# Optimization experiments

Hardware: AMD Instinct MI355X
Metric: run time of the kernel (lower is better)

The kernel has to match this reference:

```python
import jax, jax.numpy as jnp
import numpy as np

N_NODES = 50000
N_EDGES = 800000
D = 64
VOCAB = 1000
NUM_ITERS = 2
BN_EPS = 1e-5


def _bn(h, g, b):
    # BatchNorm1d in training mode: batch statistics over the edge dim, biased var
    mu = h.mean(axis=0)
    var = h.var(axis=0)
    return g * (h - mu) * jax.lax.rsqrt(var + BN_EPS) + b


def _edge_agg(x, idx_i, idx_j, W1, b1, g1, be1, W2, b2, g2, be2):
    # gather -> concat -> Linear+BN+ReLU x2 -> scatter-sum to idx_i -> degree norm
    m = jnp.concatenate([x[idx_i], x[idx_j]], axis=1)          # [E, 2D]
    h = jax.nn.relu(_bn(m @ W1 + b1, g1, be1))                  # [E, D]
    h = jax.nn.relu(_bn(h @ W2 + b2, g2, be2))                  # [E, D]
    agg = jax.ops.segment_sum(h, idx_i, num_segments=N_NODES)   # [N, D]
    deg = jax.ops.segment_sum(jnp.ones((idx_i.shape[0],), x.dtype), idx_i,
                              num_segments=N_NODES)
    deg_inv = jnp.where(deg > 0, 1.0 / deg, 0.0)
    return deg_inv[:, None] * agg


def setup_inputs() -> dict:
    key = jax.random.key(0)
    ks = jax.random.split(key, 24)
    s = 0.05
    inp = {
        'nodes': jax.random.randint(ks[0], (N_NODES,), 0, VOCAB),
        'edges': jax.random.randint(ks[1], (2, N_EDGES), 0, N_NODES),
        'emb': jax.random.normal(ks[2], (VOCAB, D), jnp.float32) * s,
        # parent aggregation MLP
        'p_W1': jax.random.normal(ks[3], (2 * D, D), jnp.float32) * s,
        'p_b1': jnp.zeros((D,), jnp.float32),
        'p_g1': jnp.ones((D,), jnp.float32),
        'p_be1': jnp.zeros((D,), jnp.float32),
        'p_W2': jax.random.normal(ks[4], (D, D), jnp.float32) * s,
        'p_b2': jnp.zeros((D,), jnp.float32),
        'p_g2': jnp.ones((D,), jnp.float32),
        'p_be2': jnp.zeros((D,), jnp.float32),
        # child aggregation MLP
        'c_W1': jax.random.normal(ks[5], (2 * D, D), jnp.float32) * s,
        'c_b1': jnp.zeros((D,), jnp.float32),
        'c_g1': jnp.ones((D,), jnp.float32),
        'c_be1': jnp.zeros((D,), jnp.float32),
        'c_W2': jax.random.normal(ks[6], (D, D), jnp.float32) * s,
        'c_b2': jnp.zeros((D,), jnp.float32),
        'c_g2': jnp.ones((D,), jnp.float32),
        'c_be2': jnp.zeros((D,), jnp.float32),
        # final aggregation (dropout = identity, eval semantics)
        'fc_W': jax.random.normal(ks[7], (3 * D, 2 * D), jnp.float32) * s,
        'fc_b': jnp.zeros((2 * D,), jnp.float32),
        'fc2_W': jax.random.normal(ks[8], (2 * D, D), jnp.float32) * s,
        'fc2_b': jnp.zeros((D,), jnp.float32),
        # Conv1d(D, 2D, kernel=1) == Linear D -> 2D
        'conv_W': jax.random.normal(ks[9], (D, 2 * D), jnp.float32) * s,
        'conv_b': jnp.zeros((2 * D,), jnp.float32),
    }
    return inp


def reference(nodes, edges, emb, p_W1, p_b1, p_g1, p_be1, p_W2, p_b2, p_g2, p_be2,
              c_W1, c_b1, c_g1, c_be1, c_W2, c_b2, c_g2, c_be2,
              fc_W, fc_b, fc2_W, fc2_b, conv_W, conv_b):
    src, dst = edges[0], edges[1]
    x = emb[nodes]                                            # [N, D]
    for _ in range(NUM_ITERS):
        # ParentAggregation: flow source_to_target -> x_i = x[dst], x_j = x[src], scatter to dst
        fi = _edge_agg(x, dst, src, p_W1, p_b1, p_g1, p_be1, p_W2, p_b2, p_g2, p_be2)
        # ChildAggregation: flow target_to_source -> x_i = x[src], x_j = x[dst], scatter to src
        fo = _edge_agg(x, src, dst, c_W1, c_b1, c_g1, c_be1, c_W2, c_b2, c_g2, c_be2)
        cat = jnp.concatenate([x, fi, fo], axis=1)            # [N, 3D]
        upd = jax.nn.relu(cat @ fc_W + fc_b) @ fc2_W + fc2_b  # [N, D]
        x = x + upd
    return x @ conv_W + conv_b                                # [N, 2D]
```

## Files before the change

kernel.cpp:

```cpp
#include <hip/hip_runtime.h>

#define NN 50000
#define NE 800000
#define BN_EPS 1e-5f
#define SCAN_T 256
#define SCAN_NB ((NN + SCAN_T - 1) / SCAN_T)

#define BKT_SH 8
#define NBKT ((NN + 255) >> 8)
#define CAP 6144
#define PCH 4096
#define NPB ((NE + PCH - 1) / PCH)

#define ST_SUM1 0
#define ST_SQ1 64
#define ST_CROSS 128
#define ST_SUM2 192
#define ST_SSQ2 256
#define ST_AGG 320

using bf16x8 = __attribute__((ext_vector_type(8))) __bf16;
using bf16x4 = __attribute__((ext_vector_type(4))) __bf16;
using floatx4 = __attribute__((ext_vector_type(4))) float;

#define MFMA16(a, b, c) __builtin_amdgcn_mfma_f32_16x16x32_bf16(a, b, c, 0, 0, 0)

__device__ __forceinline__ bf16x8 load_wfrag(const float* W, int ncols, int kb, int ct, int lane) {
  int col = ct * 16 + (lane & 15);
  int k0 = kb * 32 + ((lane >> 4) << 3);
  bf16x8 f;
#pragma unroll
  for (int j = 0; j < 8; ++j) f[j] = (__bf16)W[(k0 + j) * ncols + col];
  return f;
}

__global__ void k_setup(const int* __restrict__ nodes, const float* __restrict__ emb,
                        float* __restrict__ x, int* __restrict__ bcur) {
  int tid = blockIdx.x * blockDim.x + threadIdx.x;
  int stride = gridDim.x * blockDim.x;
  for (int idx = tid; idx < NN * 64; idx += stride)
    x[idx] = emb[nodes[idx >> 6] * 64 + (idx & 63)];
  for (int t = tid; t < 2 * NBKT; t += stride)
    bcur[t] = (t < NBKT ? t : t - NBKT) * CAP;
}

__global__ void __launch_bounds__(256) k_part(const int* __restrict__ src,
                                              const int* __restrict__ dst,
                                              int* __restrict__ bcur,
                                              unsigned int* __restrict__ stage) {
  const int dir = blockIdx.y;
  const int* key = dir ? src : dst;
  int* bc = bcur + dir * NBKT;
  unsigned int* st = stage + (size_t)dir * NBKT * CAP;
  __shared__ int lh[256];
  __shared__ int sb[256];
  __shared__ int lbase[NBKT];
  __shared__ unsigned int pay[PCH];
  const int tid = threadIdx.x;
  lh[tid] = 0;
  __syncthreads();
  const int c0 = blockIdx.x * PCH;
  const int nv = (NE - c0 < PCH) ? (NE - c0) : PCH;
  unsigned int rk[PCH / 256];
#pragma unroll
  for (int i = 0; i < PCH / 256; ++i) {
    int l = i * 256 + tid;
    if (l < nv) {
      int b = key[c0 + l] >> BKT_SH;
      int r = atomicAdd(&lh[b], 1);
      rk[i] = ((unsigned)b << 13) | (unsigned)r;
    } else {
      rk[i] = 0xFFFFFFFFu;
    }
  }
  __syncthreads();
  int cntv = lh[tid];
  sb[tid] = cntv;
  __syncthreads();
  for (int o = 1; o < 256; o <<= 1) {
    int u = (tid >= o) ? sb[tid - o] : 0;
    __syncthreads();
    sb[tid] += u;
    __syncthreads();
  }
  int excl = sb[tid] - cntv;
  __syncthreads();
  sb[tid] = excl;
  if (tid < NBKT && cntv > 0) lbase[tid] = atomicAdd(&bc[tid], cntv);
  __syncthreads();
#pragma unroll
  for (int i = 0; i < PCH / 256; ++i) {
    if (rk[i] != 0xFFFFFFFFu) {
      int e = c0 + i * 256 + tid;
      int b = (int)(rk[i] >> 13);
      int r = (int)(rk[i] & 0x1FFFu);
      unsigned int s = (unsigned)src[e], d = (unsigned)dst[e];
      pay[sb[b] + r] = dir ? ((s << 16) | d) : ((d << 16) | s);
    }
  }
  __syncthreads();
  for (int t = tid; t < nv; t += 256) {
    int lo = 0, hi = 255;
    while (lo < hi) {
      int mid = (lo + hi + 1) >> 1;
      if (sb[mid] <= t) lo = mid; else hi = mid - 1;
    }
    st[lbase[lo] + (t - sb[lo])] = pay[t];
  }
}

__global__ void __launch_bounds__(256) k_count(const int* __restrict__ bcur,
                                               const unsigned int* __restrict__ stage,
                                               int* __restrict__ cnt_d, int* __restrict__ cnt_s) {
  const int dir = blockIdx.y;
  const int b = blockIdx.x;
  int* cnt = dir ? cnt_s : cnt_d;
  const unsigned int* st = stage + (size_t)dir * NBKT * CAP + (size_t)b * CAP;
  __shared__ int lc[256];
  lc[threadIdx.x] = 0;
  __syncthreads();
  int sz = bcur[dir * NBKT + b] - b * CAP;
  for (int t = threadIdx.x; t < sz; t += 256)
    atomicAdd(&lc[(st[t] >> 16) - (b << BKT_SH)], 1);
  __syncthreads();
  int n = (b << BKT_SH) + threadIdx.x;
  if (n < NN) cnt[n] = lc[threadIdx.x];
}

__global__ void k_scan1(const int* __restrict__ cnt_d, const int* __restrict__ cnt_s,
                        int* __restrict__ off_d, int* __restrict__ off_s, int* __restrict__ btot) {
  const int* cnt = blockIdx.y ? cnt_s : cnt_d;
  int* off = blockIdx.y ? off_s : off_d;
  __shared__ int sm[SCAN_T];
  int i = blockIdx.x * SCAN_T + threadIdx.x;
  int v = (i < NN) ? cnt[i] : 0;
  sm[threadIdx.x] = v;
  __syncthreads();
  for (int o = 1; o < SCAN_T; o <<= 1) {
    int u = (threadIdx.x >= o) ? sm[threadIdx.x - o] : 0;
    __syncthreads();
    sm[threadIdx.x] += u;
    __syncthreads();
  }
  if (i < NN) off[i] = sm[threadIdx.x];
  if (threadIdx.x == SCAN_T - 1) btot[blockIdx.y * SCAN_NB + blockIdx.x] = sm[SCAN_T - 1];
}

__global__ void k_scan2(int* __restrict__ btot) {
  __shared__ int sm[SCAN_T];
  int t = threadIdx.x;
  for (int y = 0; y < 2; ++y) {
    int v = (t < SCAN_NB) ? btot[y * SCAN_NB + t] : 0;
    sm[t] = v;
    __syncthreads();
    for (int o = 1; o < SCAN_T; o <<= 1) {
      int u = (t >= o) ? sm[t - o] : 0;
      __syncthreads();
      sm[t] += u;
      __syncthreads();
    }
    if (t < SCAN_NB) btot[y * SCAN_NB + t] = sm[t] - v;
    __syncthreads();
  }
}

__global__ void k_scan3(const int* __restrict__ cnt_d, const int* __restrict__ cnt_s,
                        int* __restrict__ off_d, int* __restrict__ off_s,
                        const int* __restrict__ btot, float* __restrict__ dinv_d,
                        float* __restrict__ dinv_s) {
  const int* cnt = blockIdx.y ? cnt_s : cnt_d;
  int* off = blockIdx.y ? off_s : off_d;
  float* dinv = blockIdx.y ? dinv_s : dinv_d;
  int i = blockIdx.x * SCAN_T + threadIdx.x;
  if (i < NN) {
    int incl = off[i];
    int c = cnt[i];
    int o = incl - c + btot[blockIdx.y * SCAN_NB + blockIdx.x];
    off[i] = o;
    dinv[i] = c > 0 ? 1.0f / (float)c : 0.f;
  }
  if (i == NN - 1) off[NN] = NE;
}

__global__ void __launch_bounds__(256) k_fill2(const int* __restrict__ bcur,
                                               const unsigned int* __restrict__ stage,
                                               const int* __restrict__ off_d,
                                               const int* __restrict__ off_s,
                                               unsigned short* __restrict__ jl_d,
                                               unsigned short* __restrict__ jl_s,
                                               unsigned short* __restrict__ il_d,
                                               unsigned short* __restrict__ il_s) {
  const int dir = blockIdx.y;
  const int b = blockIdx.x;
  const int* off = dir ? off_s : off_d;
  unsigned short* jl = dir ? jl_s : jl_d;
  unsigned short* il = dir ? il_s : il_d;
  const unsigned int* st = stage + (size_t)dir * NBKT * CAP + (size_t)b * CAP;
  __shared__ int lcur[256];
  __shared__ unsigned short ljl[CAP];
  __shared__ unsigned short lil[CAP];
  int csr0 = off[b << BKT_SH];
  int n = (b << BKT_SH) + threadIdx.x;
  lcur[threadIdx.x] = (n < NN) ? off[n] - csr0 : 0;
  __syncthreads();
  int sz = bcur[dir * NBKT + b] - b * CAP;
  for (int t = threadIdx.x; t < sz; t += 256) {
    unsigned int v = st[t];
    int p = atomicAdd(&lcur[(v >> 16) - (b << BKT_SH)], 1);
    ljl[p] = (unsigned short)(v & 0xFFFFu);
    lil[p] = (unsigned short)(v >> 16);
  }
  __syncthreads();
  for (int t = threadIdx.x; t < sz; t += 256) {
    jl[csr0 + t] = ljl[t];
    il[csr0 + t] = lil[t];
  }
}

__global__ void __launch_bounds__(256) k_node_xform(
    const float* __restrict__ x, const float* __restrict__ W1,
    __bf16* __restrict__ Ab, __bf16* __restrict__ Bb,
    float* __restrict__ stats, int do_zero) {
  const int lane = threadIdx.x & 63;
  const int wid = threadIdx.x >> 6;
  __shared__ alignas(16) __bf16 xb[4][16 * 72];
  if (do_zero && blockIdx.x == 0)
    for (int t = threadIdx.x; t < 2 * ST_AGG; t += blockDim.x) stats[t] = 0.f;
  bf16x8 wfa[4][2], wfb[4][2];
#pragma unroll
  for (int ct = 0; ct < 4; ++ct)
#pragma unroll
    for (int kb = 0; kb < 2; ++kb) {
      wfa[ct][kb] = load_wfrag(W1, 64, kb, ct, lane);
      wfb[ct][kb] = load_wfrag(W1 + 64 * 64, 64, kb, ct, lane);
    }
  __bf16* vb = xb[wid];
  int wgid = (blockIdx.x * blockDim.x + threadIdx.x) >> 6;
  int nw = (gridDim.x * blockDim.x) >> 6;
  for (int tile = wgid; tile < NN / 16; tile += nw) {
#pragma unroll
    for (int t = 0; t < 16; ++t)
      vb[t * 72 + lane] = (__bf16)x[(tile * 16 + t) * 64 + lane];
    const bf16x8 a0 = *(const bf16x8*)&vb[(lane & 15) * 72 + ((lane >> 4) << 3)];
    const bf16x8 a1 = *(const bf16x8*)&vb[(lane & 15) * 72 + 32 + ((lane >> 4) << 3)];
#pragma unroll
    for (int ct = 0; ct < 4; ++ct) {
      floatx4 aA = {0.f, 0.f, 0.f, 0.f}, aB = {0.f, 0.f, 0.f, 0.f};
      aA = MFMA16(a0, wfa[ct][0], aA);
      aA = MFMA16(a1, wfa[ct][1], aA);
      aB = MFMA16(a0, wfb[ct][0], aB);
      aB = MFMA16(a1, wfb[ct][1], aB);
#pragma unroll
      for (int r = 0; r < 4; ++r) {
        int row = ((lane >> 4) << 2) + r;
        int o = (tile * 16 + row) * 64 + ct * 16 + (lane & 15);
        Ab[o] = (__bf16)aA[r];
        Bb[o] = (__bf16)aB[r];
      }
    }
  }
}

__global__ void __launch_bounds__(256) k_node_stats(
    const __bf16* __restrict__ Ap, const __bf16* __restrict__ Bp,
    const __bf16* __restrict__ Ac, const __bf16* __restrict__ Bc,
    const int* __restrict__ cnt_d, const int* __restrict__ cnt_s,
    float* __restrict__ stats) {
  const int lane = threadIdx.x & 63;
  const int g = lane >> 4, q = lane & 15;
  __shared__ float sacc[256];
  for (int t = threadIdx.x; t < 256; t += blockDim.x) sacc[t] = 0.f;
  __syncthreads();
  float sp[4] = {0, 0, 0, 0}, qp[4] = {0, 0, 0, 0};
  float sc[4] = {0, 0, 0, 0}, qc[4] = {0, 0, 0, 0};
  int wgid = (blockIdx.x * blockDim.x + threadIdx.x) >> 6;
  int nw = (gridDim.x * blockDim.x) >> 6;
  for (int ch = wgid; ch < NN / 4; ch += nw) {
    int n = ch * 4 + g;
    float wd = (float)cnt_d[n];
    float ws = (float)cnt_s[n];
    bf16x4 ap = *(const bf16x4*)(Ap + n * 64 + 4 * q);
    bf16x4 bp = *(const bf16x4*)(Bp + n * 64 + 4 * q);
    bf16x4 ac = *(const bf16x4*)(Ac + n * 64 + 4 * q);
    bf16x4 bc = *(const bf16x4*)(Bc + n * 64 + 4 * q);
#pragma unroll
    for (int k = 0; k < 4; ++k) {
      float a = (float)ap[k], b = (float)bp[k], c = (float)ac[k], d = (float)bc[k];
      sp[k] += wd * a + ws * b;
      qp[k] += wd * a * a + ws * b * b;
      sc[k] += ws * c + wd * d;
      qc[k] += ws * c * c + wd * d * d;
    }
  }
#pragma unroll
  for (int k = 0; k < 4; ++k) {
    sp[k] += __shfl_xor(sp[k], 16); sp[k] += __shfl_xor(sp[k], 32);
    qp[k] += __shfl_xor(qp[k], 16); qp[k] += __shfl_xor(qp[k], 32);
    sc[k] += __shfl_xor(sc[k], 16); sc[k] += __shfl_xor(sc[k], 32);
    qc[k] += __shfl_xor(qc[k], 16); qc[k] += __shfl_xor(qc[k], 32);
  }
  if (lane < 16) {
#pragma unroll
    for (int k = 0; k < 4; ++k) {
      atomicAdd(&sacc[4 * q + k], sp[k]);
      atomicAdd(&sacc[64 + 4 * q + k], qp[k]);
      atomicAdd(&sacc[128 + 4 * q + k], sc[k]);
      atomicAdd(&sacc[192 + 4 * q + k], qc[k]);
    }
  }
  __syncthreads();
  for (int t = threadIdx.x; t < 256; t += blockDim.x) {
    int dstoff = (t < 128) ? t : ST_AGG + (t - 128);
    atomicAdd(&stats[dstoff], sacc[t]);
  }
}

__global__ void __launch_bounds__(256) k_cross_csr2(
    const unsigned short* __restrict__ il, const unsigned short* __restrict__ jl,
    const __bf16* __restrict__ Ap, const __bf16* __restrict__ Bp,
    const __bf16* __restrict__ Ac, const __bf16* __restrict__ Bc,
    float* __restrict__ stats) {
  const int lane = threadIdx.x & 63;
  const int c8 = lane & 7, e8 = lane >> 3;
  __shared__ float sacc[128];
  for (int t = threadIdx.x; t < 128; t += blockDim.x) sacc[t] = 0.f;
  __syncthreads();
  float cp[8] = {0, 0, 0, 0, 0, 0, 0, 0}, cc[8] = {0, 0, 0, 0, 0, 0, 0, 0};
  int wgid = (blockIdx.x * blockDim.x + threadIdx.x) >> 6;
  int nw = (gridDim.x * blockDim.x) >> 6;
  for (int tile = wgid; tile < NE / 16; tile += nw) {
    int e0 = tile * 16;
    int iv = (int)il[e0 + (lane & 15)];
    int jv = (int)jl[e0 + (lane & 15)];
#pragma unroll
    for (int r = 0; r < 2; ++r) {
      int ee = r * 8 + e8;
      int i = __shfl(iv, ee);
      int j = __shfl(jv, ee);
      bf16x8 ap = *(const bf16x8*)(Ap + (size_t)i * 64 + c8 * 8);
      bf16x8 bp = *(const bf16x8*)(Bp + (size_t)j * 64 + c8 * 8);
      bf16x8 ac = *(const bf16x8*)(Ac + (size_t)j * 64 + c8 * 8);
      bf16x8 bc = *(const bf16x8*)(Bc + (size_t)i * 64 + c8 * 8);
#pragma unroll
      for (int k = 0; k < 8; ++k) {
        cp[k] += (float)ap[k] * (float)bp[k];
        cc[k] += (float)ac[k] * (float)bc[k];
      }
    }
  }
#pragma unroll
  for (int k = 0; k < 8; ++k) {
    cp[k] += __shfl_xor(cp[k], 8);  cp[k] += __shfl_xor(cp[k], 16); cp[k] += __shfl_xor(cp[k], 32);
    cc[k] += __shfl_xor(cc[k], 8);  cc[k] += __shfl_xor(cc[k], 16); cc[k] += __shfl_xor(cc[k], 32);
  }
  if (lane < 8) {
#pragma unroll
    for (int k = 0; k < 8; ++k) {
      atomicAdd(&sacc[lane * 8 + k], cp[k]);
      atomicAdd(&sacc[64 + lane * 8 + k], cc[k]);
    }
  }
  __syncthreads();
  for (int t = threadIdx.x; t < 128; t += blockDim.x) {
    int dstoff = (t < 64) ? (ST_CROSS + t) : (ST_AGG + ST_CROSS + (t - 64));
    atomicAdd(&stats[dstoff], sacc[t]);
  }
}

__global__ void __launch_bounds__(256) k_edge_stats_csr2(
    const unsigned short* __restrict__ il, const unsigned short* __restrict__ jl,
    const __bf16* __restrict__ Ap, const __bf16* __restrict__ Bp,
    const __bf16* __restrict__ Ac, const __bf16* __restrict__ Bc,
    const float* __restrict__ pg1, const float* __restrict__ pbe1,
    const float* __restrict__ cg1, const float* __restrict__ cbe1,
    const float* __restrict__ pW2, const float* __restrict__ cW2,
    float* __restrict__ stats) {
  const int lane = threadIdx.x & 63;
  const int wid = threadIdx.x >> 6;
  const int g = lane >> 4, q = lane & 15;
  const int c8 = lane & 7;
  const int e8 = lane >> 3;
  __shared__ alignas(16) __bf16 vbuf[4][2][16 * 72];
  __shared__ float sred[256];
  float s1p[8], t1p[8], s1c[8], t1c[8];
#pragma unroll
  for (int k = 0; k < 8; ++k) {
    int c = c8 * 8 + k;
    float mu = stats[ST_SUM1 + c] * (1.f / NE);
    float var = (stats[ST_SQ1 + c] + 2.f * stats[ST_CROSS + c]) * (1.f / NE) - mu * mu;
    float s = pg1[c] * rsqrtf(var + BN_EPS);
    s1p[k] = s;
    t1p[k] = pbe1[c] - mu * s;
    mu = stats[ST_AGG + ST_SUM1 + c] * (1.f / NE);
    var = (stats[ST_AGG + ST_SQ1 + c] + 2.f * stats[ST_AGG + ST_CROSS + c]) * (1.f / NE) - mu * mu;
    s = cg1[c] * rsqrtf(var + BN_EPS);
    s1c[k] = s;
    t1c[k] = cbe1[c] - mu * s;
  }
  bf16x8 wfp[4][2], wfc[4][2];
#pragma unroll
  for (int ct = 0; ct < 4; ++ct)
#pragma unroll
    for (int kb = 0; kb < 2; ++kb) {
      wfp[ct][kb] = load_wfrag(pW2, 64, kb, ct, lane);
      wfc[ct][kb] = load_wfrag(cW2, 64, kb, ct, lane);
    }
  float sump[4] = {0, 0, 0, 0}, ssqp[4] = {0, 0, 0, 0};
  float sumc[4] = {0, 0, 0, 0}, ssqc[4] = {0, 0, 0, 0};
  __bf16* vbp = vbuf[wid][0];
  __bf16* vbc = vbuf[wid][1];
  int wgid = (blockIdx.x * blockDim.x + threadIdx.x) >> 6;
  int nw = (gridDim.x * blockDim.x) >> 6;
  for (int tile = wgid; tile < NE / 16; tile += nw) {
    int e0 = tile * 16;
    int iv = (int)il[e0 + q];
    int jv = (int)jl[e0 + q];
#pragma unroll
    for (int r = 0; r < 2; ++r) {
      int ee = r * 8 + e8;
      int i = __shfl(iv, ee);
      int j = __shfl(jv, ee);
      bf16x8 ap = *(const bf16x8*)(Ap + (size_t)i * 64 + c8 * 8);
      bf16x8 bp = *(const bf16x8*)(Bp + (size_t)j * 64 + c8 * 8);
      bf16x8 ac = *(const bf16x8*)(Ac + (size_t)j * 64 + c8 * 8);
      bf16x8 bc = *(const bf16x8*)(Bc + (size_t)i * 64 + c8 * 8);
      bf16x8 vp, vc;
#pragma unroll
      for (int k = 0; k < 8; ++k) {
        vp[k] = (__bf16)fmaxf(s1p[k] * ((float)ap[k] + (float)bp[k]) + t1p[k], 0.f);
        vc[k] = (__bf16)fmaxf(s1c[k] * ((float)ac[k] + (float)bc[k]) + t1c[k], 0.f);
      }
      *(bf16x8*)&vbp[ee * 72 + c8 * 8] = vp;
      *(bf16x8*)&vbc[ee * 72 + c8 * 8] = vc;
    }
    const bf16x8 a0p = *(const bf16x8*)&vbp[q * 72 + g * 8];
    const bf16x8 a1p = *(const bf16x8*)&vbp[q * 72 + 32 + g * 8];
    const bf16x8 a0c = *(const bf16x8*)&vbc[q * 72 + g * 8];
    const bf16x8 a1c = *(const bf16x8*)&vbc[q * 72 + 32 + g * 8];
#pragma unroll
    for (int ct = 0; ct < 4; ++ct) {
      floatx4 accp = {0.f, 0.f, 0.f, 0.f}, accc = {0.f, 0.f, 0.f, 0.f};
      accp = MFMA16(a0p, wfp[ct][0], accp);
      accp = MFMA16(a1p, wfp[ct][1], accp);
      accc = MFMA16(a0c, wfc[ct][0], accc);
      accc = MFMA16(a1c, wfc[ct][1], accc);
#pragma unroll
      for (int r = 0; r < 4; ++r) {
        float hp = accp[r], hc = accc[r];
        sump[ct] += hp;
        ssqp[ct] += hp * hp;
        sumc[ct] += hc;
        ssqc[ct] += hc * hc;
      }
    }
  }
  for (int t = threadIdx.x; t < 256; t += blockDim.x) sred[t] = 0.f;
  __syncthreads();
#pragma unroll
  for (int ct = 0; ct < 4; ++ct) {
    atomicAdd(&sred[ct * 16 + q], sump[ct]);
    atomicAdd(&sred[64 + ct * 16 + q], ssqp[ct]);
    atomicAdd(&sred[128 + ct * 16 + q], sumc[ct]);
    atomicAdd(&sred[192 + ct * 16 + q], ssqc[ct]);
  }
  __syncthreads();
  for (int t = threadIdx.x; t < 256; t += blockDim.x) {
    int dstoff;
    if (t < 64) dstoff = ST_SUM2 + t;
    else if (t < 128) dstoff = ST_SSQ2 + (t - 64);
    else if (t < 192) dstoff = ST_AGG + ST_SUM2 + (t - 128);
    else dstoff = ST_AGG + ST_SSQ2 + (t - 192);
    atomicAdd(&stats[dstoff], sred[t]);
  }
}

__global__ void __launch_bounds__(256) k_scatter_fused(
    const int* __restrict__ off, const float* __restrict__ dinv,
    const unsigned short* __restrict__ jl, const __bf16* __restrict__ A_,
    const __bf16* __restrict__ B_, const float* __restrict__ g1,
    const float* __restrict__ be1, const float* __restrict__ g2,
    const float* __restrict__ be2, const float* __restrict__ W2,
    const float* __restrict__ stats, int sbase, float* __restrict__ outb) {
  const int lane = threadIdx.x & 63;
  const int wid = threadIdx.x >> 6;
  const int g = lane >> 4, q = lane & 15;
  __shared__ alignas(16) __bf16 vbuf[4][16 * 72];
  float s1v[4], t1v[4];
#pragma unroll
  for (int k = 0; k < 4; ++k) {
    int c = 4 * q + k;
    float mu = stats[sbase + ST_SUM1 + c] * (1.f / NE);
    float var = (stats[sbase + ST_SQ1 + c] + 2.f * stats[sbase + ST_CROSS + c]) * (1.f / NE) - mu * mu;
    float s = g1[c] * rsqrtf(var + BN_EPS);
    s1v[k] = s;
    t1v[k] = be1[c] - mu * s;
  }
  float s2v[4], t2v[4];
#pragma unroll
  for (int ct = 0; ct < 4; ++ct) {
    int c = ct * 16 + q;
    float mu = stats[sbase + ST_SUM2 + c] * (1.f / NE);
    float var = stats[sbase + ST_SSQ2 + c] * (1.f / NE) - mu * mu;
    float s = g2[c] * rsqrtf(var + BN_EPS);
    s2v[ct] = s;
    t2v[ct] = be2[c] - mu * s;
  }
  bf16x8 wf[4][2];
#pragma unroll
  for (int ct = 0; ct < 4; ++ct)
#pragma unroll
    for (int kb = 0; kb < 2; ++kb) wf[ct][kb] = load_wfrag(W2, 64, kb, ct, lane);
  __bf16* vb = vbuf[wid];
  int wgid = (blockIdx.x * blockDim.x + threadIdx.x) >> 6;
  int nw = (gridDim.x * blockDim.x) >> 6;
  for (int n = wgid; n < NN; n += nw) {
    int p0 = off[n], p1 = off[n + 1];
    bf16x4 a4 = *(const bf16x4*)(A_ + (size_t)n * 64 + 4 * q);
    float ha[4];
#pragma unroll
    for (int k = 0; k < 4; ++k) ha[k] = (float)a4[k];
    float oacc[4] = {0.f, 0.f, 0.f, 0.f};
    for (int pt = p0; pt < p1; pt += 16) {
      int m = p1 - pt;
      if (m > 16) m = 16;
      int jj = (lane < m) ? (int)jl[pt + lane] : 0;
#pragma unroll
      for (int t = 0; t < 4; ++t) {
        int et = t * 4 + g;
        int j = __shfl(jj, et);
        bf16x4 b4 = *(const bf16x4*)(B_ + (size_t)j * 64 + 4 * q);
        bf16x4 v4;
#pragma unroll
        for (int k = 0; k < 4; ++k)
          v4[k] = (__bf16)fmaxf(s1v[k] * (ha[k] + (float)b4[k]) + t1v[k], 0.f);
        *(bf16x4*)&vb[et * 72 + 4 * q] = v4;
      }
      const bf16x8 a0 = *(const bf16x8*)&vb[q * 72 + g * 8];
      const bf16x8 a1 = *(const bf16x8*)&vb[q * 72 + 32 + g * 8];
#pragma unroll
      for (int ct = 0; ct < 4; ++ct) {
        floatx4 acc = {0.f, 0.f, 0.f, 0.f};
        acc = MFMA16(a0, wf[ct][0], acc);
        acc = MFMA16(a1, wf[ct][1], acc);
#pragma unroll
        for (int r = 0; r < 4; ++r)
          if (g * 4 + r < m) oacc[ct] += fmaxf(s2v[ct] * acc[r] + t2v[ct], 0.f);
      }
    }
#pragma unroll
    for (int ct = 0; ct < 4; ++ct) {
      oacc[ct] += __shfl_xor(oacc[ct], 16);
      oacc[ct] += __shfl_xor(oacc[ct], 32);
    }
    float val = (g == 0) ? oacc[0] : (g == 1) ? oacc[1] : (g == 2) ? oacc[2] : oacc[3];
    outb[(size_t)n * 64 + lane] = dinv[n] * val;
  }
}

__global__ void __launch_bounds__(256) k_node_update(
    float* __restrict__ x, const float* __restrict__ fi, const float* __restrict__ fo,
    const float* __restrict__ fcW, const float* __restrict__ fcb,
    const float* __restrict__ fc2W, const float* __restrict__ fc2b) {
  const int lane = threadIdx.x & 63;
  const int wid = threadIdx.x >> 6;
  __shared__ alignas(16) __bf16 cat[16 * 200];
  __shared__ alignas(16) __bf16 v2[16 * 136];
  bf16x8 wf1[2][6];
#pragma unroll
  for (int c = 0; c < 2; ++c) {
    int ct = 2 * wid + c;
#pragma unroll
    for (int kb = 0; kb < 6; ++kb) wf1[c][kb] = load_wfrag(fcW, 128, kb, ct, lane);
  }
  bf16x8 wf2[4];
#pragma unroll
  for (int kb = 0; kb < 4; ++kb) wf2[kb] = load_wfrag(fc2W, 64, kb, wid, lane);
  float fcbv[2];
#pragma unroll
  for (int c = 0; c < 2; ++c) fcbv[c] = fcb[(2 * wid + c) * 16 + (lane & 15)];
  float fc2bv = fc2b[wid * 16 + (lane & 15)];

  for (int tile = blockIdx.x; tile < NN / 16; tile += gridDim.x) {
#pragma unroll
    for (int r = 0; r < 4; ++r) {
      int rr = wid * 4 + r;
      int n = tile * 16 + rr;
      cat[rr * 200 + lane] = (__bf16)x[n * 64 + lane];
      cat[rr * 200 + 64 + lane] = (__bf16)fi[n * 64 + lane];
      cat[rr * 200 + 128 + lane] = (__bf16)fo[n * 64 + lane];
    }
    __syncthreads();
    floatx4 acc0 = {0.f, 0.f, 0.f, 0.f}, acc1 = {0.f, 0.f, 0.f, 0.f};
#pragma unroll
    for (int kb = 0; kb < 6; ++kb) {
      bf16x8 af = *(const bf16x8*)&cat[(lane & 15) * 200 + kb * 32 + ((lane >> 4) << 3)];
      acc0 = MFMA16(af, wf1[0][kb], acc0);
      acc1 = MFMA16(af, wf1[1][kb], acc1);
    }
#pragma unroll
    for (int r = 0; r < 4; ++r) {
      int row = ((lane >> 4) << 2) + r;
      v2[row * 136 + (2 * wid) * 16 + (lane & 15)] = (__bf16)fmaxf(acc0[r] + fcbv[0], 0.f);
      v2[row * 136 + (2 * wid + 1) * 16 + (lane & 15)] = (__bf16)fmaxf(acc1[r] + fcbv[1], 0.f);
    }
    __syncthreads();
    floatx4 a2 = {0.f, 0.f, 0.f, 0.f};
#pragma unroll
    for (int kb = 0; kb < 4; ++kb) {
      bf16x8 af = *(const bf16x8*)&v2[(lane & 15) * 136 + kb * 32 + ((lane >> 4) << 3)];
      a2 = MFMA16(af, wf2[kb], a2);
    }
#pragma unroll
    for (int r = 0; r < 4; ++r) {
      int row = ((lane >> 4) << 2) + r;
      int n = tile * 16 + row;
      x[n * 64 + wid * 16 + (lane & 15)] += a2[r] + fc2bv;
    }
    __syncthreads();
  }
}

__global__ void __launch_bounds__(256) k_conv(const float* __restrict__ x,
                                              const float* __restrict__ convW,
                                              const float* __restrict__ convb,
                                              float* __restrict__ out) {
  const int lane = threadIdx.x & 63;
  const int wid = threadIdx.x >> 6;
  const int q = lane & 15, g = lane >> 4;
  __shared__ alignas(16) __bf16 xh[4][16 * 72];
  __shared__ alignas(16) __bf16 xl[4][16 * 72];
  bf16x8 wf[8][2];
#pragma unroll
  for (int ct = 0; ct < 8; ++ct)
#pragma unroll
    for (int kb = 0; kb < 2; ++kb) wf[ct][kb] = load_wfrag(convW, 128, kb, ct, lane);
  float bv[8];
#pragma unroll
  for (int ct = 0; ct < 8; ++ct) bv[ct] = convb[ct * 16 + q];
  __bf16* vh = xh[wid];
  __bf16* vl = xl[wid];
  int wgid = (blockIdx.x * blockDim.x + threadIdx.x) >> 6;
  int nw = (gridDim.x * blockDim.x) >> 6;
  for (int tile = wgid; tile < NN / 16; tile += nw) {
#pragma unroll
    for (int t = 0; t < 16; ++t) {
      float xv = x[(tile * 16 + t) * 64 + lane];
      __bf16 h = (__bf16)xv;
      vh[t * 72 + lane] = h;
      vl[t * 72 + lane] = (__bf16)(xv - (float)h);
    }
    const bf16x8 h0 = *(const bf16x8*)&vh[q * 72 + (g << 3)];
    const bf16x8 h1 = *(const bf16x8*)&vh[q * 72 + 32 + (g << 3)];
    const bf16x8 l0 = *(const bf16x8*)&vl[q * 72 + (g << 3)];
    const bf16x8 l1 = *(const bf16x8*)&vl[q * 72 + 32 + (g << 3)];
#pragma unroll
    for (int ct = 0; ct < 8; ++ct) {
      floatx4 acc = {0.f, 0.f, 0.f, 0.f};
      acc = MFMA16(l0, wf[ct][0], acc);
      acc = MFMA16(l1, wf[ct][1], acc);
      acc = MFMA16(h0, wf[ct][0], acc);
      acc = MFMA16(h1, wf[ct][1], acc);
#pragma unroll
      for (int r = 0; r < 4; ++r) {
        int row = (g << 2) + r;
        out[(size_t)(tile * 16 + row) * 128 + ct * 16 + q] = acc[r] + bv[ct];
      }
    }
  }
}

extern "C" void kernel_launch(void* const* d_in, const int* in_sizes, int n_in,
                              void* d_out, int out_size, void* d_ws, size_t ws_size,
                              hipStream_t stream) {
  const int* nodes = (const int*)d_in[0];
  const int* edges = (const int*)d_in[1];
  const int* src = edges;
  const int* dst = edges + NE;
  const float* emb = (const float*)d_in[2];
  const float* pW1 = (const float*)d_in[3];
  const float* pg1 = (const float*)d_in[5];
  const float* pbe1 = (const float*)d_in[6];
  const float* pW2 = (const float*)d_in[7];
  const float* pg2 = (const float*)d_in[9];
  const float* pbe2 = (const float*)d_in[10];
  const float* cW1 = (const float*)d_in[11];
  const float* cg1 = (const float*)d_in[13];
  const float* cbe1 = (const float*)d_in[14];
  const float* cW2 = (const float*)d_in[15];
  const float* cg2 = (const float*)d_in[17];
  const float* cbe2 = (const float*)d_in[18];
  const float* fcW = (const float*)d_in[19];
  const float* fcb = (const float*)d_in[20];
  const float* fc2W = (const float*)d_in[21];
  const float* fc2b = (const float*)d_in[22];
  const float* convW = (const float*)d_in[23];
  const float* convb = (const float*)d_in[24];
  float* out = (float*)d_out;

  char* w = (char*)d_ws;
  auto alloc = [&](size_t bytes) {
    char* p = w;
    w += (bytes + 255) & ~(size_t)255;
    return p;
  };
  float* x = (float*)alloc((size_t)NN * 64 * 4);
  __bf16* Ap = (__bf16*)alloc((size_t)NN * 64 * 2);
  __bf16* Bp = (__bf16*)alloc((size_t)NN * 64 * 2);
  __bf16* Ac = (__bf16*)alloc((size_t)NN * 64 * 2);
  __bf16* Bc = (__bf16*)alloc((size_t)NN * 64 * 2);
  float* fi = (float*)alloc((size_t)NN * 64 * 4);
  float* fo = (float*)alloc((size_t)NN * 64 * 4);
  unsigned short* jl_d = (unsigned short*)alloc((size_t)NE * 2);
  unsigned short* jl_s = (unsigned short*)alloc((size_t)NE * 2);
  unsigned short* il_d = (unsigned short*)alloc((size_t)NE * 2);
  unsigned short* il_s = (unsigned short*)alloc((size_t)NE * 2);
  int* off_d = (int*)alloc((size_t)(NN + 1) * 4);
  int* off_s = (int*)alloc((size_t)(NN + 1) * 4);
  int* cnt_d = (int*)alloc((size_t)NN * 4);
  int* cnt_s = (int*)alloc((size_t)NN * 4);
  float* dinv_d = (float*)alloc((size_t)NN * 4);
  float* dinv_s = (float*)alloc((size_t)NN * 4);
  float* stats = (float*)alloc(2 * ST_AGG * 4);
  int* btot = (int*)alloc(2 * SCAN_NB * 4);
  int* bcur = (int*)alloc((size_t)2 * NBKT * 4);
  unsigned int* stage = (unsigned int*)alloc((size_t)2 * NBKT * CAP * 4);

  k_setup<<<1024, 256, 0, stream>>>(nodes, emb, x, bcur);
  k_part<<<dim3(NPB, 2), 256, 0, stream>>>(src, dst, bcur, stage);
  k_count<<<dim3(NBKT, 2), 256, 0, stream>>>(bcur, stage, cnt_d, cnt_s);
  k_scan1<<<dim3(SCAN_NB, 2), SCAN_T, 0, stream>>>(cnt_d, cnt_s, off_d, off_s, btot);
  k_scan2<<<1, SCAN_T, 0, stream>>>(btot);
  k_scan3<<<dim3(SCAN_NB, 2), SCAN_T, 0, stream>>>(cnt_d, cnt_s, off_d, off_s, btot,
                                                   dinv_d, dinv_s);
  k_fill2<<<dim3(NBKT, 2), 256, 0, stream>>>(bcur, stage, off_d, off_s, jl_d, jl_s,
                                             il_d, il_s);

  for (int it = 0; it < 2; ++it) {
    k_node_xform<<<784, 256, 0, stream>>>(x, pW1, Ap, Bp, stats, 1);
    k_node_xform<<<784, 256, 0, stream>>>(x, cW1, Ac, Bc, stats, 0);
    k_node_stats<<<256, 256, 0, stream>>>(Ap, Bp, Ac, Bc, cnt_d, cnt_s, stats);
    k_cross_csr2<<<2048, 256, 0, stream>>>(il_d, jl_d, Ap, Bp, Ac, Bc, stats);
    k_edge_stats_csr2<<<2048, 256, 0, stream>>>(il_d, jl_d, Ap, Bp, Ac, Bc, pg1, pbe1,
                                                cg1, cbe1, pW2, cW2, stats);
    k_scatter_fused<<<2048, 256, 0, stream>>>(off_d, dinv_d, jl_d, Ap, Bp, pg1, pbe1,
                                              pg2, pbe2, pW2, stats, 0, fi);
    k_scatter_fused<<<2048, 256, 0, stream>>>(off_s, dinv_s, jl_s, Ac, Bc, cg1, cbe1,
                                              cg2, cbe2, cW2, stats, ST_AGG, fo);
    k_node_update<<<3125, 256, 0, stream>>>(x, fi, fo, fcW, fcb, fc2W, fc2b);
  }
  k_conv<<<784, 256, 0, stream>>>(x, convW, convb, out);
}
```

Baseline: 856.7 us.

## Interleave per-node projections so edge kernels gather two 256-byte rows

The four per-node bf16 projection arrays are packed into two interleaved arrays, iP and jP. iP holds Ap and Bc, jP holds Bp and Ac, each row 128 wide. Edge kernels indexed by i and j now fetch one contiguous 256-byte row per endpoint instead of four separate 128-byte rows from four arrays. Lane mapping in the cross-stats and edge-stats kernels changes to 16 columns by 4 edges. The goal is fewer scattered gather transactions and better cache-line use. The scatter kernels now read strided rows, which wastes half of each fetched line.

```diff
diff --git a/kernel.cpp b/kernel.cpp
--- a/kernel.cpp
+++ b/kernel.cpp
@@ -219,7 +219,7 @@
 
 __global__ void __launch_bounds__(256) k_node_xform(
     const float* __restrict__ x, const float* __restrict__ W1,
-    __bf16* __restrict__ Ab, __bf16* __restrict__ Bb,
+    __bf16* __restrict__ Aout, int astr, __bf16* __restrict__ Bout, int bstr,
     float* __restrict__ stats, int do_zero) {
   const int lane = threadIdx.x & 63;
   const int wid = threadIdx.x >> 6;
@@ -253,17 +253,17 @@
 #pragma unroll
       for (int r = 0; r < 4; ++r) {
         int row = ((lane >> 4) << 2) + r;
-        int o = (tile * 16 + row) * 64 + ct * 16 + (lane & 15);
-        Ab[o] = (__bf16)aA[r];
-        Bb[o] = (__bf16)aB[r];
+        int n = tile * 16 + row;
+        int col = ct * 16 + (lane & 15);
+        Aout[(size_t)n * astr + col] = (__bf16)aA[r];
+        Bout[(size_t)n * bstr + col] = (__bf16)aB[r];
       }
     }
   }
 }
 
 __global__ void __launch_bounds__(256) k_node_stats(
-    const __bf16* __restrict__ Ap, const __bf16* __restrict__ Bp,
-    const __bf16* __restrict__ Ac, const __bf16* __restrict__ Bc,
+    const __bf16* __restrict__ iP, const __bf16* __restrict__ jP,
     const int* __restrict__ cnt_d, const int* __restrict__ cnt_s,
     float* __restrict__ stats) {
   const int lane = threadIdx.x & 63;
@@ -279,10 +279,10 @@
     int n = ch * 4 + g;
     float wd = (float)cnt_d[n];
     float ws = (float)cnt_s[n];
-    bf16x4 ap = *(const bf16x4*)(Ap + n * 64 + 4 * q);
-    bf16x4 bp = *(const bf16x4*)(Bp + n * 64 + 4 * q);
-    bf16x4 ac = *(const bf16x4*)(Ac + n * 64 + 4 * q);
-    bf16x4 bc = *(const bf16x4*)(Bc + n * 64 + 4 * q);
+    bf16x4 ap = *(const bf16x4*)(iP + (size_t)n * 128 + 4 * q);
+    bf16x4 bp = *(const bf16x4*)(jP + (size_t)n * 128 + 4 * q);
+    bf16x4 ac = *(const bf16x4*)(jP + (size_t)n * 128 + 64 + 4 * q);
+    bf16x4 bc = *(const bf16x4*)(iP + (size_t)n * 128 + 64 + 4 * q);
 #pragma unroll
     for (int k = 0; k < 4; ++k) {
       float a = (float)ap[k], b = (float)bp[k], c = (float)ac[k], d = (float)bc[k];
@@ -315,49 +315,43 @@
   }
 }
 
-__global__ void __launch_bounds__(256) k_cross_csr2(
+__global__ void __launch_bounds__(256) k_cross_csr3(
     const unsigned short* __restrict__ il, const unsigned short* __restrict__ jl,
-    const __bf16* __restrict__ Ap, const __bf16* __restrict__ Bp,
-    const __bf16* __restrict__ Ac, const __bf16* __restrict__ Bc,
+    const __bf16* __restrict__ iP, const __bf16* __restrict__ jP,
     float* __restrict__ stats) {
   const int lane = threadIdx.x & 63;
-  const int c8 = lane & 7, e8 = lane >> 3;
+  const int c16 = lane & 15, r4 = lane >> 4;
   __shared__ float sacc[128];
   for (int t = threadIdx.x; t < 128; t += blockDim.x) sacc[t] = 0.f;
   __syncthreads();
-  float cp[8] = {0, 0, 0, 0, 0, 0, 0, 0}, cc[8] = {0, 0, 0, 0, 0, 0, 0, 0};
+  float acc[8] = {0, 0, 0, 0, 0, 0, 0, 0};
   int wgid = (blockIdx.x * blockDim.x + threadIdx.x) >> 6;
   int nw = (gridDim.x * blockDim.x) >> 6;
   for (int tile = wgid; tile < NE / 16; tile += nw) {
     int e0 = tile * 16;
-    int iv = (int)il[e0 + (lane & 15)];
-    int jv = (int)jl[e0 + (lane & 15)];
-#pragma unroll
-    for (int r = 0; r < 2; ++r) {
-      int ee = r * 8 + e8;
+    int iv = (int)il[e0 + c16];
+    int jv = (int)jl[e0 + c16];
+#pragma unroll
+    for (int r = 0; r < 4; ++r) {
+      int ee = r * 4 + r4;
       int i = __shfl(iv, ee);
       int j = __shfl(jv, ee);
-      bf16x8 ap = *(const bf16x8*)(Ap + (size_t)i * 64 + c8 * 8);
-      bf16x8 bp = *(const bf16x8*)(Bp + (size_t)j * 64 + c8 * 8);
-      bf16x8 ac = *(const bf16x8*)(Ac + (size_t)j * 64 + c8 * 8);
-      bf16x8 bc = *(const bf16x8*)(Bc + (size_t)i * 64 + c8 * 8);
-#pragma unroll
-      for (int k = 0; k < 8; ++k) {
-        cp[k] += (float)ap[k] * (float)bp[k];
-        cc[k] += (float)ac[k] * (float)bc[k];
-      }
+      bf16x8 av = *(const bf16x8*)(iP + (size_t)i * 128 + c16 * 8);
+      bf16x8 bv = *(const bf16x8*)(jP + (size_t)j * 128 + c16 * 8);
+#pragma unroll
+      for (int k = 0; k < 8; ++k) acc[k] += (float)av[k] * (float)bv[k];
     }
   }
 #pragma unroll
   for (int k = 0; k < 8; ++k) {
-    cp[k] += __shfl_xor(cp[k], 8);  cp[k] += __shfl_xor(cp[k], 16); cp[k] += __shfl_xor(cp[k], 32);
-    cc[k] += __shfl_xor(cc[k], 8);  cc[k] += __shfl_xor(cc[k], 16); cc[k] += __shfl_xor(cc[k], 32);
-  }
-  if (lane < 8) {
+    acc[k] += __shfl_xor(acc[k], 16);
+    acc[k] += __shfl_xor(acc[k], 32);
+  }
+  if (lane < 16) {
 #pragma unroll
     for (int k = 0; k < 8; ++k) {
-      atomicAdd(&sacc[lane * 8 + k], cp[k]);
-      atomicAdd(&sacc[64 + lane * 8 + k], cc[k]);
+      int dst = (c16 < 8) ? (c16 * 8 + k) : (64 + (c16 - 8) * 8 + k);
+      atomicAdd(&sacc[dst], acc[k]);
     }
   }
   __syncthreads();
@@ -367,10 +361,9 @@
   }
 }
 
-__global__ void __launch_bounds__(256) k_edge_stats_csr2(
+__global__ void __launch_bounds__(256) k_edge_stats_csr3(
     const unsigned short* __restrict__ il, const unsigned short* __restrict__ jl,
-    const __bf16* __restrict__ Ap, const __bf16* __restrict__ Bp,
-    const __bf16* __restrict__ Ac, const __bf16* __restrict__ Bc,
+    const __bf16* __restrict__ iP, const __bf16* __restrict__ jP,
     const float* __restrict__ pg1, const float* __restrict__ pbe1,
     const float* __restrict__ cg1, const float* __restrict__ cbe1,
     const float* __restrict__ pW2, const float* __restrict__ cW2,
@@ -378,24 +371,24 @@
   const int lane = threadIdx.x & 63;
   const int wid = threadIdx.x >> 6;
   const int g = lane >> 4, q = lane & 15;
-  const int c8 = lane & 7;
-  const int e8 = lane >> 3;
+  const int c16 = lane & 15, r4 = lane >> 4;
   __shared__ alignas(16) __bf16 vbuf[4][2][16 * 72];
   __shared__ float sred[256];
-  float s1p[8], t1p[8], s1c[8], t1c[8];
-#pragma unroll
-  for (int k = 0; k < 8; ++k) {
-    int c = c8 * 8 + k;
-    float mu = stats[ST_SUM1 + c] * (1.f / NE);
-    float var = (stats[ST_SQ1 + c] + 2.f * stats[ST_CROSS + c]) * (1.f / NE) - mu * mu;
-    float s = pg1[c] * rsqrtf(var + BN_EPS);
-    s1p[k] = s;
-    t1p[k] = pbe1[c] - mu * s;
-    mu = stats[ST_AGG + ST_SUM1 + c] * (1.f / NE);
-    var = (stats[ST_AGG + ST_SQ1 + c] + 2.f * stats[ST_AGG + ST_CROSS + c]) * (1.f / NE) - mu * mu;
-    s = cg1[c] * rsqrtf(var + BN_EPS);
-    s1c[k] = s;
-    t1c[k] = cbe1[c] - mu * s;
+  float s1[8], t1[8];
+  {
+    int sb2 = (c16 < 8) ? 0 : ST_AGG;
+    const float* gg = (c16 < 8) ? pg1 : cg1;
+    const float* bb = (c16 < 8) ? pbe1 : cbe1;
+    int cbase = (c16 & 7) * 8;
+#pragma unroll
+    for (int k = 0; k < 8; ++k) {
+      int c = cbase + k;
+      float mu = stats[sb2 + ST_SUM1 + c] * (1.f / NE);
+      float var = (stats[sb2 + ST_SQ1 + c] + 2.f * stats[sb2 + ST_CROSS + c]) * (1.f / NE) - mu * mu;
+      float s = gg[c] * rsqrtf(var + BN_EPS);
+      s1[k] = s;
+      t1[k] = bb[c] - mu * s;
+    }
   }
   bf16x8 wfp[4][2], wfc[4][2];
 #pragma unroll
@@ -409,29 +402,26 @@
   float sumc[4] = {0, 0, 0, 0}, ssqc[4] = {0, 0, 0, 0};
   __bf16* vbp = vbuf[wid][0];
   __bf16* vbc = vbuf[wid][1];
+  const int cbase = (c16 & 7) * 8;
   int wgid = (blockIdx.x * blockDim.x + threadIdx.x) >> 6;
   int nw = (gridDim.x * blockDim.x) >> 6;
   for (int tile = wgid; tile < NE / 16; tile += nw) {
     int e0 = tile * 16;
-    int iv = (int)il[e0 + q];
-    int jv = (int)jl[e0 + q];
-#pragma unroll
-    for (int r = 0; r < 2; ++r) {
-      int ee = r * 8 + e8;
+    int iv = (int)il[e0 + c16];
+    int jv = (int)jl[e0 + c16];
+#pragma unroll
+    for (int r = 0; r < 4; ++r) {
+      int ee = r * 4 + r4;
       int i = __shfl(iv, ee);
       int j = __shfl(jv, ee);
-      bf16x8 ap = *(const bf16x8*)(Ap + (size_t)i * 64 + c8 * 8);
-      bf16x8 bp = *(const bf16x8*)(Bp + (size_t)j * 64 + c8 * 8);
-      bf16x8 ac = *(const bf16x8*)(Ac + (size_t)j * 64 + c8 * 8);
-      bf16x8 bc = *(const bf16x8*)(Bc + (size_t)i * 64 + c8 * 8);
-      bf16x8 vp, vc;
-#pragma unroll
-      for (int k = 0; k < 8; ++k) {
-        vp[k] = (__bf16)fmaxf(s1p[k] * ((float)ap[k] + (float)bp[k]) + t1p[k], 0.f);
-        vc[k] = (__bf16)fmaxf(s1c[k] * ((float)ac[k] + (float)bc[k]) + t1c[k], 0.f);
-      }
-      *(bf16x8*)&vbp[ee * 72 + c8 * 8] = vp;
-      *(bf16x8*)&vbc[ee * 72 + c8 * 8] = vc;
+      bf16x8 av = *(const bf16x8*)(iP + (size_t)i * 128 + c16 * 8);
+      bf16x8 bv = *(const bf16x8*)(jP + (size_t)j * 128 + c16 * 8);
+      bf16x8 v;
+#pragma unroll
+      for (int k = 0; k < 8; ++k)
+        v[k] = (__bf16)fmaxf(s1[k] * ((float)av[k] + (float)bv[k]) + t1[k], 0.f);
+      __bf16* dst = (c16 < 8) ? &vbp[ee * 72 + cbase] : &vbc[ee * 72 + cbase];
+      *(bf16x8*)dst = v;
     }
     const bf16x8 a0p = *(const bf16x8*)&vbp[q * 72 + g * 8];
     const bf16x8 a1p = *(const bf16x8*)&vbp[q * 72 + 32 + g * 8];
@@ -476,8 +466,8 @@
 
 __global__ void __launch_bounds__(256) k_scatter_fused(
     const int* __restrict__ off, const float* __restrict__ dinv,
-    const unsigned short* __restrict__ jl, const __bf16* __restrict__ A_,
-    const __bf16* __restrict__ B_, const float* __restrict__ g1,
+    const unsigned short* __restrict__ jl, const __bf16* __restrict__ A_, int astr,
+    const __bf16* __restrict__ B_, int bstr, const float* __restrict__ g1,
     const float* __restrict__ be1, const float* __restrict__ g2,
     const float* __restrict__ be2, const float* __restrict__ W2,
     const float* __restrict__ stats, int sbase, float* __restrict__ outb) {
@@ -515,7 +505,7 @@
   int nw = (gridDim.x * blockDim.x) >> 6;
   for (int n = wgid; n < NN; n += nw) {
     int p0 = off[n], p1 = off[n + 1];
-    bf16x4 a4 = *(const bf16x4*)(A_ + (size_t)n * 64 + 4 * q);
+    bf16x4 a4 = *(const bf16x4*)(A_ + (size_t)n * astr + 4 * q);
     float ha[4];
 #pragma unroll
     for (int k = 0; k < 4; ++k) ha[k] = (float)a4[k];
@@ -528,7 +518,7 @@
       for (int t = 0; t < 4; ++t) {
         int et = t * 4 + g;
         int j = __shfl(jj, et);
-        bf16x4 b4 = *(const bf16x4*)(B_ + (size_t)j * 64 + 4 * q);
+        bf16x4 b4 = *(const bf16x4*)(B_ + (size_t)j * bstr + 4 * q);
         bf16x4 v4;
 #pragma unroll
         for (int k = 0; k < 4; ++k)
@@ -704,10 +694,8 @@
     return p;
   };
   float* x = (float*)alloc((size_t)NN * 64 * 4);
-  __bf16* Ap = (__bf16*)alloc((size_t)NN * 64 * 2);
-  __bf16* Bp = (__bf16*)alloc((size_t)NN * 64 * 2);
-  __bf16* Ac = (__bf16*)alloc((size_t)NN * 64 * 2);
-  __bf16* Bc = (__bf16*)alloc((size_t)NN * 64 * 2);
+  __bf16* iP = (__bf16*)alloc((size_t)NN * 128 * 2);
+  __bf16* jP = (__bf16*)alloc((size_t)NN * 128 * 2);
   float* fi = (float*)alloc((size_t)NN * 64 * 4);
   float* fo = (float*)alloc((size_t)NN * 64 * 4);
   unsigned short* jl_d = (unsigned short*)alloc((size_t)NE * 2);
@@ -736,16 +724,17 @@
                                              il_d, il_s);
 
   for (int it = 0; it < 2; ++it) {
-    k_node_xform<<<784, 256, 0, stream>>>(x, pW1, Ap, Bp, stats, 1);
-    k_node_xform<<<784, 256, 0, stream>>>(x, cW1, Ac, Bc, stats, 0);
-    k_node_stats<<<256, 256, 0, stream>>>(Ap, Bp, Ac, Bc, cnt_d, cnt_s, stats);
-    k_cross_csr2<<<2048, 256, 0, stream>>>(il_d, jl_d, Ap, Bp, Ac, Bc, stats);
-    k_edge_stats_csr2<<<2048, 256, 0, stream>>>(il_d, jl_d, Ap, Bp, Ac, Bc, pg1, pbe1,
+    k_node_xform<<<784, 256, 0, stream>>>(x, pW1, iP, 128, jP, 128, stats, 1);
+    k_node_xform<<<784, 256, 0, stream>>>(x, cW1, jP + 64, 128, iP + 64, 128, stats, 0);
+    k_node_stats<<<256, 256, 0, stream>>>(iP, jP, cnt_d, cnt_s, stats);
+    k_cross_csr3<<<2048, 256, 0, stream>>>(il_d, jl_d, iP, jP, stats);
+    k_edge_stats_csr3<<<2048, 256, 0, stream>>>(il_d, jl_d, iP, jP, pg1, pbe1,
                                                 cg1, cbe1, pW2, cW2, stats);
-    k_scatter_fused<<<2048, 256, 0, stream>>>(off_d, dinv_d, jl_d, Ap, Bp, pg1, pbe1,
-                                              pg2, pbe2, pW2, stats, 0, fi);
-    k_scatter_fused<<<2048, 256, 0, stream>>>(off_s, dinv_s, jl_s, Ac, Bc, cg1, cbe1,
-                                              cg2, cbe2, cW2, stats, ST_AGG, fo);
+    k_scatter_fused<<<2048, 256, 0, stream>>>(off_d, dinv_d, jl_d, iP, 128, jP, 128,
+                                              pg1, pbe1, pg2, pbe2, pW2, stats, 0, fi);
+    k_scatter_fused<<<2048, 256, 0, stream>>>(off_s, dinv_s, jl_s, jP + 64, 128,
+                                              iP + 64, 128, cg1, cbe1, cg2, cbe2, cW2,
+                                              stats, ST_AGG, fo);
     k_node_update<<<3125, 256, 0, stream>>>(x, fi, fo, fcW, fcb, fc2W, fc2b);
   }
   k_conv<<<784, 256, 0, stream>>>(x, convW, convb, out);
```

Measured after the change: 819.0 us. -4.4%, faster.
